# Optimization experiments

Hardware: AMD Instinct MI355X
Metric: run time of the kernel (lower is better)

## Reference

```python
import jax, jax.numpy as jnp
import numpy as np

D_HEAD = 64
KV_HEADS = 8
Q_HEADS = 32
ROPE_BASE = 10000.0


def rope(x):
    # x: (B, S, H, D); pairs are interleaved along last dim, matching torch view(...,D//2,2)
    B, S, H, D = x.shape
    inv_freq = 1.0 / (ROPE_BASE ** (jnp.arange(0, D, 2, dtype=jnp.float32) / D))
    theta = jnp.arange(S, dtype=jnp.float32)[:, None] * inv_freq[None, :]  # (S, D/2)
    cos = jnp.cos(theta)[None, :, None, :]
    sin = jnp.sin(theta)[None, :, None, :]
    xf = x.astype(jnp.float32).reshape(B, S, H, D // 2, 2)
    x1, x2 = xf[..., 0], xf[..., 1]
    out = jnp.stack((x1 * cos - x2 * sin, x1 * sin + x2 * cos), axis=-1)
    return out.reshape(B, S, H, D).astype(x.dtype)


def setup_inputs() -> dict:
    key = jax.random.key(0)
    ks = jax.random.split(key, 5)
    B, S, D = 2, 2048, 2048
    scale = 1.0 / np.sqrt(D)
    return {
        "x": jax.random.normal(ks[0], (B, S, D), dtype=jnp.float32),
        "Wq": jax.random.normal(ks[1], (Q_HEADS * D_HEAD, D), dtype=jnp.float32) * scale,
        "Wk": jax.random.normal(ks[2], (KV_HEADS * D_HEAD, D), dtype=jnp.float32) * scale,
        "Wv": jax.random.normal(ks[3], (KV_HEADS * D_HEAD, D), dtype=jnp.float32) * scale,
        "Wo": jax.random.normal(ks[4], (D, D), dtype=jnp.float32) * scale,
    }


def reference(x, Wq, Wk, Wv, Wo):
    B, S, D = x.shape
    G = Q_HEADS // KV_HEADS  # query heads per kv head

    Q = (x @ Wq.T).reshape(B, S, Q_HEADS, D_HEAD)
    K = (x @ Wk.T).reshape(B, S, KV_HEADS, D_HEAD)
    V = (x @ Wv.T).reshape(B, S, KV_HEADS, D_HEAD)

    Q = rope(Q)
    K = rope(K)

    # (B, KV, G, S, Dh): group g of kv head h corresponds to q head h*G+g,
    # exactly matching repeat_interleave of K/V along head dim.
    Q = Q.transpose(0, 2, 1, 3).reshape(B, KV_HEADS, G, S, D_HEAD)
    K = K.transpose(0, 2, 1, 3)  # (B, KV, S, Dh)
    V = V.transpose(0, 2, 1, 3)

    scores = jnp.einsum("bkgsd,bktd->bkgst", Q, K) / np.sqrt(D_HEAD).astype(np.float32)
    causal_mask = jnp.tril(jnp.ones((S, S), dtype=bool))
    scores = jnp.where(causal_mask, scores, -jnp.inf)
    probs = jax.nn.softmax(scores, axis=-1)
    attn = jnp.einsum("bkgst,bktd->bkgsd", probs, V)

    attn = attn.reshape(B, Q_HEADS, S, D_HEAD).transpose(0, 2, 1, 3).reshape(B, S, D)
    return attn @ Wo.T
```

## Files before the change

### kernel.cpp

```cpp
#include <hip/hip_runtime.h>
#include <stdint.h>

#define S_LEN   2048
#define D_MODEL 2048
#define DKV     512

typedef __attribute__((ext_vector_type(8))) short short8;
typedef __attribute__((ext_vector_type(4))) float f32x4;

__device__ static inline unsigned short f2bf(float f) {
  unsigned u = __builtin_bit_cast(unsigned, f);
  u += 0x7FFFu + ((u >> 16) & 1u);
  return (unsigned short)(u >> 16);
}
__device__ static inline float bf2f(unsigned short h) {
  return __builtin_bit_cast(float, ((unsigned)h) << 16);
}
__device__ static inline unsigned packtrunc2(float f0, float f1) {
  return __builtin_amdgcn_perm(__builtin_bit_cast(unsigned, f1),
                               __builtin_bit_cast(unsigned, f0), 0x07060302u);
}

__device__ static inline void gload_lds16(const void* g, void* lds) {
  __builtin_amdgcn_global_load_lds((const __attribute__((address_space(1))) void*)g,
                                   (__attribute__((address_space(3))) void*)lds,
                                   16, 0, 0);
}

template <int N>
__device__ __forceinline__ void wait_vm() {
  if constexpr (N == 8)      asm volatile("s_waitcnt vmcnt(8)" ::: "memory");
  else if constexpr (N == 6) asm volatile("s_waitcnt vmcnt(6)" ::: "memory");
  else if constexpr (N == 4) asm volatile("s_waitcnt vmcnt(4)" ::: "memory");
  else if constexpr (N == 3) asm volatile("s_waitcnt vmcnt(3)" ::: "memory");
  else                       asm volatile("s_waitcnt vmcnt(0)" ::: "memory");
}

__global__ __launch_bounds__(256) void cvt_all_kernel(
    const float* __restrict__ x, const float* __restrict__ wq, const float* __restrict__ wk,
    const float* __restrict__ wv, const float* __restrict__ wo,
    unsigned short* __restrict__ xb, unsigned short* __restrict__ wqb,
    unsigned short* __restrict__ wkb, unsigned short* __restrict__ wvb,
    unsigned short* __restrict__ wob, float2* __restrict__ tab) {
  if (blockIdx.x >= 9216) {
    const int idx = (blockIdx.x - 9216) * 256 + threadIdx.x;
    const int s = idx >> 5, i = idx & 31;
    const float inv = exp2f(-0.41524101186091903f * (float)i);
    const float th  = (float)s * inv;
    tab[idx] = make_float2(cosf(th), sinf(th));
    return;
  }
  int i = blockIdx.x * 256 + threadIdx.x;
  const float* s; unsigned short* d;
  if (i < 1048576)      { s = x;  d = xb;  }
  else if (i < 1572864) { s = wq; d = wqb; i -= 1048576; }
  else if (i < 1703936) { s = wk; d = wkb; i -= 1572864; }
  else if (i < 1835008) { s = wv; d = wvb; i -= 1703936; }
  else                  { s = wo; d = wob; i -= 1835008; }
  const float4 a = ((const float4*)s)[i * 2];
  const float4 b = ((const float4*)s)[i * 2 + 1];
  unsigned short u[8] = {f2bf(a.x), f2bf(a.y), f2bf(a.z), f2bf(a.w),
                         f2bf(b.x), f2bf(b.y), f2bf(b.z), f2bf(b.w)};
  *(uint4*)(d + (size_t)i * 8) = *(const uint4*)u;
}

template <int BM, int CMODE, int RMODE, typename CT>
__device__ __forceinline__ void gemm_deep_body(
    const unsigned short* __restrict__ A, int lda,
    const unsigned short* __restrict__ B, int ldb,
    CT* __restrict__ C, int ldc, int m0, int n0, unsigned short* ldsu,
    const float2* __restrict__ tab) {
  constexpr int MI = BM / 32;
  constexpr int NI = 4;
  constexpr int A_BYTES = BM * 64;
  constexpr int B_BYTES = 256 * 64;
  constexpr int TILE_BYTES = A_BYTES + B_BYTES;
  constexpr int AL = BM / 128;
  constexpr int LOADS = AL + 2;
  constexpr int VMS = 2 * LOADS;

  const int tid  = threadIdx.x;
  const int lane = tid & 63;
  const int w    = tid >> 6;
  const int wm   = w >> 2;
  const int wn   = w & 3;
  const int lcol = lane & 15;
  const int lq   = lane >> 4;
  char* const ldsb = (char*)ldsu;

  const int sl   = (lane & 7) ^ (lane >> 3);
  const int colg = (sl & 3) * 8;
  const unsigned short* gA[AL];
  const unsigned short* gB[2];
#pragma unroll
  for (int L = 0; L < AL; ++L) {
    const int r = 2 * (L * 64 + w * 8 + (lane >> 3)) + (sl >> 2);
    gA[L] = A + (size_t)(m0 + r) * lda + colg;
  }
#pragma unroll
  for (int L = 0; L < 2; ++L) {
    const int r = 2 * (L * 64 + w * 8 + (lane >> 3)) + (sl >> 2);
    gB[L] = B + (size_t)(n0 + r) * ldb + colg;
  }

  auto stage = [&](int tt) {
    char* const sb = ldsb + (tt & 3) * TILE_BYTES;
#pragma unroll
    for (int L = 0; L < AL; ++L)
      gload_lds16(gA[L] + tt * 32, sb + L * 8192 + w * 1024);
#pragma unroll
    for (int L = 0; L < 2; ++L)
      gload_lds16(gB[L] + tt * 32, sb + A_BYTES + L * 8192 + w * 1024);
  };

  const int sR    = (((lcol & 1) << 2) | lq) ^ ((lcol >> 1) & 7);
  const int rdoff = (lcol >> 1) * 128 + sR * 16;

  f32x4 acc[MI][NI] = {};

  auto compute_tile = [&](char* buf) {
    short8 af[MI], bfr[NI];
#pragma unroll
    for (int mi = 0; mi < MI; ++mi)
      af[mi] = *(const short8*)(buf + wm * (MI * 1024) + mi * 1024 + rdoff);
#pragma unroll
    for (int ni = 0; ni < NI; ++ni)
      bfr[ni] = *(const short8*)(buf + A_BYTES + wn * 4096 + ni * 1024 + rdoff);
    __builtin_amdgcn_s_setprio(1);
#pragma unroll
    for (int mi = 0; mi < MI; ++mi)
#pragma unroll
      for (int ni = 0; ni < NI; ++ni)
        acc[mi][ni] = __builtin_amdgcn_mfma_f32_16x16x32_bf16(af[mi], bfr[ni], acc[mi][ni], 0, 0, 0);
    __builtin_amdgcn_s_setprio(0);
  };

  stage(0); stage(1); stage(2);

#define GPHASE(T, VMW, DOSTG)                          \
  do {                                                 \
    wait_vm<VMW>();                                    \
    __builtin_amdgcn_s_barrier();                      \
    asm volatile("" ::: "memory");                     \
    __builtin_amdgcn_sched_barrier(0);                 \
    if (DOSTG) stage((T) + 3);                         \
    compute_tile(ldsb + ((T) & 3) * TILE_BYTES);       \
  } while (0)

  for (int t4 = 0; t4 < 15; ++t4) {
    const int t = t4 * 4;
    GPHASE(t + 0, VMS, true);
    GPHASE(t + 1, VMS, true);
    GPHASE(t + 2, VMS, true);
    GPHASE(t + 3, VMS, true);
  }
  GPHASE(60, VMS,   true);
  GPHASE(61, VMS,   false);
  GPHASE(62, LOADS, false);
  GPHASE(63, 0,     false);
#undef GPHASE

  if constexpr (CMODE == 1) {
    unsigned short* ldsT = ldsu;
    __syncthreads();
#pragma unroll
    for (int mi = 0; mi < MI; ++mi)
#pragma unroll
      for (int ni = 0; ni < NI; ++ni) {
        const int c  = wn * 64 + ni * 16 + lcol;
        const int rl = wm * (MI * 16) + mi * 16 + lq * 4;
        unsigned short u4[4] = {f2bf(acc[mi][ni][0]), f2bf(acc[mi][ni][1]),
                                f2bf(acc[mi][ni][2]), f2bf(acc[mi][ni][3])};
        *(uint2*)&ldsT[c * 264 + rl] = *(const uint2*)u4;
      }
    __syncthreads();
    const int bI   = m0 >> 11;
    const int s0   = m0 & 2047;
    const int half = lane >> 5;
    const int sl32 = lane & 31;
#pragma unroll
    for (int it = 0; it < 16; ++it) {
      const int d = it * 16 + w * 2 + half;
      const uint4 v = *(const uint4*)&ldsT[d * 264 + sl32 * 8];
      *(uint4*)&C[((size_t)(bI * 512 + n0 + d)) * 2048 + s0 + sl32 * 8] = v;
    }
  } else {
#pragma unroll
    for (int mi = 0; mi < MI; ++mi)
#pragma unroll
      for (int ni = 0; ni < NI; ++ni)
#pragma unroll
        for (int r = 0; r < 4; ++r) {
          const int row = m0 + wm * (MI * 16) + mi * 16 + lq * 4 + r;
          const int col = n0 + wn * 64 + ni * 16 + lcol;
          float v = acc[mi][ni][r];
          if constexpr (RMODE > 0) {
            const float p = __shfl_xor(v, 1);
            const int d = col & 63;
            const float2 cs = tab[(row & (S_LEN - 1)) * 32 + (d >> 1)];
            v = (d & 1) ? (p * cs.y + v * cs.x) : (v * cs.x - p * cs.y);
            if constexpr (RMODE == 2) v *= 0.1803368801111244f;
          }
          if constexpr (CMODE == 2) {
            C[(size_t)row * ldc + col] = v;
          } else {
            C[(size_t)row * ldc + col] = f2bf(v);
          }
        }
  }
}

__global__ __launch_bounds__(512, 2) void qkv_gemm_kernel(
    const unsigned short* __restrict__ x,
    const unsigned short* __restrict__ Wq, const unsigned short* __restrict__ Wk,
    const unsigned short* __restrict__ Wv,
    unsigned short* __restrict__ Qo, unsigned short* __restrict__ Ko,
    unsigned short* __restrict__ Vt, const float2* __restrict__ tab) {
  extern __shared__ __align__(16) unsigned short lds[];
  const int bid = blockIdx.x;
  const int xcd = bid & 7, l = bid >> 3;
  const int gm = xcd >> 2, gn = xcd & 3;
  const int mt = gm * 8 + (l & 7);
  const int nt = gn * 3 + (l >> 3);
  const int m0 = mt * 256;
  if (nt < 8)
    gemm_deep_body<256, 0, 2, unsigned short>(x, D_MODEL, Wq, D_MODEL, Qo, D_MODEL, m0, nt * 256, lds, tab);
  else if (nt < 10)
    gemm_deep_body<256, 0, 1, unsigned short>(x, D_MODEL, Wk, D_MODEL, Ko, DKV, m0, (nt - 8) * 256, lds, tab);
  else
    gemm_deep_body<256, 1, 0, unsigned short>(x, D_MODEL, Wv, D_MODEL, Vt, DKV, m0, (nt - 10) * 256, lds, tab);
}

__global__ __launch_bounds__(512, 2) void oproj_gemm_kernel(
    const unsigned short* __restrict__ A, const unsigned short* __restrict__ Wo,
    float* __restrict__ C) {
  extern __shared__ __align__(16) unsigned short lds[];
  const int bid = blockIdx.x;
  const int xcd = bid & 7, l = bid >> 3;
  const int gm = xcd >> 1, gn = xcd & 1;
  const int mt = gm * 8 + (l & 7);
  const int nt = gn * 4 + (l >> 3);
  gemm_deep_body<128, 2, 0, float>(A, D_MODEL, Wo, D_MODEL, C, D_MODEL, mt * 128, nt * 256, lds,
                                   (const float2*)nullptr);
}

__global__ __launch_bounds__(256, 2) void attn_kernel(const unsigned short* __restrict__ Q,
                                                      const unsigned short* __restrict__ K,
                                                      const unsigned short* __restrict__ Vt,
                                                      unsigned short* __restrict__ O) {
  const int hq = blockIdx.y;
  const int bb = blockIdx.z;
  const int hk = hq >> 2;
  const int tid  = threadIdx.x;
  const int lane = tid & 63;
  const int w    = tid >> 6;
  const int lcol = lane & 15;
  const int lq   = lane >> 4;
  const int trow = tid >> 2;
  const int tq   = (tid & 3) * 16;

  const int X = blockIdx.x;
  const int qt[4] = {X, 15 - X, 16 + X, 31 - X};

  __shared__ unsigned short Ks[64 * 72];
  __shared__ unsigned short Vts[64 * 72];
  __shared__ unsigned short Ps[4][64 * 72];

  const int prow = w * 16 + lcol;

  uint4 kp0, kp1, vp0, vp1;
  {
    const unsigned short* gk = K + ((size_t)(bb * S_LEN + trow)) * DKV + hk * 64 + tq;
    kp0 = *(const uint4*)gk; kp1 = *(const uint4*)(gk + 8);
    const unsigned short* gv = Vt + ((size_t)(bb * DKV + hk * 64 + trow)) * S_LEN + tq;
    vp0 = *(const uint4*)gv; vp1 = *(const uint4*)(gv + 8);
  }

#pragma unroll
  for (int j = 0; j < 4; ++j) {
    const unsigned short* g = Q + ((size_t)(bb * S_LEN + qt[j] * 64 + trow)) * D_MODEL + hq * 64 + tq;
    *(uint4*)&Ps[j][trow * 72 + tq]     = *(const uint4*)g;
    *(uint4*)&Ps[j][trow * 72 + tq + 8] = *(const uint4*)(g + 8);
  }
  asm volatile("s_waitcnt lgkmcnt(0)" ::: "memory");

  short8 qf[4][2];
#pragma unroll
  for (int j = 0; j < 4; ++j)
#pragma unroll
    for (int ks = 0; ks < 2; ++ks)
      qf[j][ks] = *(const short8*)&Ps[j][prow * 72 + ks * 32 + lq * 8];

  f32x4 Oacc[4][4] = {};
  float lacc[4] = {0.f, 0.f, 0.f, 0.f};

  const int tmax = qt[3];
  for (int t = 0; t <= tmax; ++t) {
    __syncthreads();
    *(uint4*)&Ks[trow * 72 + tq]      = kp0;
    *(uint4*)&Ks[trow * 72 + tq + 8]  = kp1;
    *(uint4*)&Vts[trow * 72 + tq]     = vp0;
    *(uint4*)&Vts[trow * 72 + tq + 8] = vp1;
    if (t < tmax) {
      const int t1 = (t + 1) * 64;
      const unsigned short* gk = K + ((size_t)(bb * S_LEN + t1 + trow)) * DKV + hk * 64 + tq;
      kp0 = *(const uint4*)gk; kp1 = *(const uint4*)(gk + 8);
      const unsigned short* gv = Vt + ((size_t)(bb * DKV + hk * 64 + trow)) * S_LEN + t1 + tq;
      vp0 = *(const uint4*)gv; vp1 = *(const uint4*)(gv + 8);
    }
    __syncthreads();

    bool act[4];
#pragma unroll
    for (int j = 0; j < 4; ++j) act[j] = (t <= qt[j]);

    f32x4 S[4][4] = {};
#pragma unroll
    for (int ks = 0; ks < 2; ++ks)
#pragma unroll
      for (int nt = 0; nt < 4; ++nt) {
        const short8 kf = *(const short8*)&Ks[(nt * 16 + lcol) * 72 + ks * 32 + lq * 8];
#pragma unroll
        for (int j = 0; j < 4; ++j)
          if (act[j])
            S[j][nt] = __builtin_amdgcn_mfma_f32_16x16x32_bf16(kf, qf[j][ks], S[j][nt], 0, 0, 0);
      }

#pragma unroll
    for (int j = 0; j < 4; ++j) {
      if (!act[j]) continue;
      if (t == qt[j]) {
        const int qrow = qt[j] * 64 + prow;
#pragma unroll
        for (int nt = 0; nt < 4; ++nt)
#pragma unroll
          for (int r = 0; r < 4; ++r) {
            const int key = t * 64 + nt * 16 + lq * 4 + r;
            if (key > qrow) S[j][nt][r] = -1e30f;
          }
      }
#pragma unroll
      for (int nt = 0; nt < 4; ++nt) {
        const float p0 = __builtin_amdgcn_exp2f(S[j][nt][0]);
        const float p1 = __builtin_amdgcn_exp2f(S[j][nt][1]);
        const float p2 = __builtin_amdgcn_exp2f(S[j][nt][2]);
        const float p3 = __builtin_amdgcn_exp2f(S[j][nt][3]);
        lacc[j] += (p0 + p1) + (p2 + p3);
        unsigned u2[2] = {packtrunc2(p0, p1), packtrunc2(p2, p3)};
        *(uint2*)&Ps[j][prow * 72 + nt * 16 + lq * 4] = *(const uint2*)u2;
      }
    }
    asm volatile("s_waitcnt lgkmcnt(0)" ::: "memory");

#pragma unroll
    for (int ks = 0; ks < 2; ++ks) {
      short8 pf[4];
#pragma unroll
      for (int j = 0; j < 4; ++j)
        if (act[j]) pf[j] = *(const short8*)&Ps[j][prow * 72 + ks * 32 + lq * 8];
#pragma unroll
      for (int dt = 0; dt < 4; ++dt) {
        const short8 vf = *(const short8*)&Vts[(dt * 16 + lcol) * 72 + ks * 32 + lq * 8];
#pragma unroll
        for (int j = 0; j < 4; ++j)
          if (act[j])
            Oacc[j][dt] = __builtin_amdgcn_mfma_f32_16x16x32_bf16(vf, pf[j], Oacc[j][dt], 0, 0, 0);
      }
    }
  }

#pragma unroll
  for (int j = 0; j < 4; ++j) {
    float l = lacc[j];
    l += __shfl_xor(l, 16);
    l += __shfl_xor(l, 32);
    const float inv = 1.0f / l;
    const int qrow = qt[j] * 64 + prow;
#pragma unroll
    for (int dt = 0; dt < 4; ++dt) {
      unsigned short u[4] = {f2bf(Oacc[j][dt][0] * inv), f2bf(Oacc[j][dt][1] * inv),
                             f2bf(Oacc[j][dt][2] * inv), f2bf(Oacc[j][dt][3] * inv)};
      *(uint2*)&O[(size_t)(bb * S_LEN + qrow) * D_MODEL + hq * 64 + dt * 16 + lq * 4] =
          *(const uint2*)u;
    }
  }
}

extern "C" void kernel_launch(void* const* d_in, const int* in_sizes, int n_in,
                              void* d_out, int out_size, void* d_ws, size_t ws_size,
                              hipStream_t stream) {
  const float* x  = (const float*)d_in[0];
  const float* Wq = (const float*)d_in[1];
  const float* Wk = (const float*)d_in[2];
  const float* Wv = (const float*)d_in[3];
  const float* Wo = (const float*)d_in[4];
  float* out = (float*)d_out;

  unsigned short* Qb  = (unsigned short*)d_ws;
  unsigned short* Kb  = Qb  + (size_t)4096 * 2048;
  unsigned short* Vtg = Kb  + (size_t)4096 * 512;
  unsigned short* Ab  = Vtg + (size_t)1024 * 2048;
  unsigned short* xb  = Ab  + (size_t)4096 * 2048;
  unsigned short* Wqb = xb  + (size_t)4096 * 2048;
  unsigned short* Wkb = Wqb + (size_t)2048 * 2048;
  unsigned short* Wvb = Wkb + (size_t)512 * 2048;
  unsigned short* Wob = Wvb + (size_t)512 * 2048;
  float2* tab = (float2*)(Wob + (size_t)2048 * 2048);

  static bool attr_set = false;
  if (!attr_set) {
    hipFuncSetAttribute(reinterpret_cast<const void*>(qkv_gemm_kernel),
                        hipFuncAttributeMaxDynamicSharedMemorySize, 135168);
    hipFuncSetAttribute(reinterpret_cast<const void*>(oproj_gemm_kernel),
                        hipFuncAttributeMaxDynamicSharedMemorySize, 98304);
    attr_set = true;
  }

  cvt_all_kernel<<<9472, 256, 0, stream>>>(x, Wq, Wk, Wv, Wo, xb, Wqb, Wkb, Wvb, Wob, tab);

  qkv_gemm_kernel<<<192, 512, 135168, stream>>>(xb, Wqb, Wkb, Wvb, Qb, Kb, Vtg, tab);
  attn_kernel<<<dim3(8, 32, 2), 256, 0, stream>>>(Qb, Kb, Vtg, Ab);
  oproj_gemm_kernel<<<256, 512, 98304, stream>>>(Ab, Wob, out);
}
```

Measured before the change: 275.4 us.

## Shrink QKV and O-proj GEMM tiles to 128x128 with 256-thread blocks

Replaces the 256x256 (QKV) and 128x256 (O-proj) GEMM tiles with one 128x128 tile specialisation using 4 waves and 64 KB of LDS. It launches 768 and 512 blocks instead of 192 and 256, and remaps the XCD-aware block swizzle to match. The goal is to fill all CUs of the MI355X, since the old grids left many idle, and to let more blocks co-reside. In exchange, each K-slice gets less data reuse, which means more global and LDS traffic per FLOP.

Result: slower. 283.0 us (+2.8%).

```diff
diff --git a/kernel.cpp b/kernel.cpp
--- a/kernel.cpp
+++ b/kernel.cpp
@@ -64,73 +64,61 @@
   *(uint4*)(d + (size_t)i * 8) = *(const uint4*)u;
 }
 
-template <int BM, int CMODE, int RMODE, typename CT>
-__device__ __forceinline__ void gemm_deep_body(
+template <int CMODE, int RMODE, typename CT>
+__device__ __forceinline__ void gemm128_deep(
     const unsigned short* __restrict__ A, int lda,
     const unsigned short* __restrict__ B, int ldb,
-    CT* __restrict__ C, int ldc, int m0, int n0, unsigned short* ldsu,
-    const float2* __restrict__ tab) {
-  constexpr int MI = BM / 32;
-  constexpr int NI = 4;
-  constexpr int A_BYTES = BM * 64;
-  constexpr int B_BYTES = 256 * 64;
-  constexpr int TILE_BYTES = A_BYTES + B_BYTES;
-  constexpr int AL = BM / 128;
-  constexpr int LOADS = AL + 2;
-  constexpr int VMS = 2 * LOADS;
-
+    CT* __restrict__ C, int ldc, int m0, int n0,
+    unsigned short* ldsu, const float2* __restrict__ tab) {
+  constexpr int LOADS = 4;
+  constexpr int VMS   = 8;
   const int tid  = threadIdx.x;
   const int lane = tid & 63;
   const int w    = tid >> 6;
-  const int wm   = w >> 2;
-  const int wn   = w & 3;
+  const int wm   = w >> 1, wn = w & 1;
   const int lcol = lane & 15;
   const int lq   = lane >> 4;
   char* const ldsb = (char*)ldsu;
 
   const int sl   = (lane & 7) ^ (lane >> 3);
   const int colg = (sl & 3) * 8;
-  const unsigned short* gA[AL];
+  const unsigned short* gA[2];
   const unsigned short* gB[2];
 #pragma unroll
-  for (int L = 0; L < AL; ++L) {
-    const int r = 2 * (L * 64 + w * 8 + (lane >> 3)) + (sl >> 2);
+  for (int L = 0; L < 2; ++L) {
+    const int r = 2 * (L * 32 + w * 8 + (lane >> 3)) + (sl >> 2);
     gA[L] = A + (size_t)(m0 + r) * lda + colg;
-  }
-#pragma unroll
-  for (int L = 0; L < 2; ++L) {
-    const int r = 2 * (L * 64 + w * 8 + (lane >> 3)) + (sl >> 2);
     gB[L] = B + (size_t)(n0 + r) * ldb + colg;
   }
 
   auto stage = [&](int tt) {
-    char* const sb = ldsb + (tt & 3) * TILE_BYTES;
-#pragma unroll
-    for (int L = 0; L < AL; ++L)
-      gload_lds16(gA[L] + tt * 32, sb + L * 8192 + w * 1024);
+    char* const sb = ldsb + (tt & 3) * 16384;
 #pragma unroll
     for (int L = 0; L < 2; ++L)
-      gload_lds16(gB[L] + tt * 32, sb + A_BYTES + L * 8192 + w * 1024);
+      gload_lds16(gA[L] + tt * 32, sb + L * 4096 + w * 1024);
+#pragma unroll
+    for (int L = 0; L < 2; ++L)
+      gload_lds16(gB[L] + tt * 32, sb + 8192 + L * 4096 + w * 1024);
   };
 
   const int sR    = (((lcol & 1) << 2) | lq) ^ ((lcol >> 1) & 7);
   const int rdoff = (lcol >> 1) * 128 + sR * 16;
 
-  f32x4 acc[MI][NI] = {};
+  f32x4 acc[4][4] = {};
 
   auto compute_tile = [&](char* buf) {
-    short8 af[MI], bfr[NI];
-#pragma unroll
-    for (int mi = 0; mi < MI; ++mi)
-      af[mi] = *(const short8*)(buf + wm * (MI * 1024) + mi * 1024 + rdoff);
-#pragma unroll
-    for (int ni = 0; ni < NI; ++ni)
-      bfr[ni] = *(const short8*)(buf + A_BYTES + wn * 4096 + ni * 1024 + rdoff);
+    short8 af[4], bfr[4];
+#pragma unroll
+    for (int mi = 0; mi < 4; ++mi)
+      af[mi] = *(const short8*)(buf + wm * 4096 + mi * 1024 + rdoff);
+#pragma unroll
+    for (int ni = 0; ni < 4; ++ni)
+      bfr[ni] = *(const short8*)(buf + 8192 + wn * 4096 + ni * 1024 + rdoff);
     __builtin_amdgcn_s_setprio(1);
 #pragma unroll
-    for (int mi = 0; mi < MI; ++mi)
-#pragma unroll
-      for (int ni = 0; ni < NI; ++ni)
+    for (int mi = 0; mi < 4; ++mi)
+#pragma unroll
+      for (int ni = 0; ni < 4; ++ni)
         acc[mi][ni] = __builtin_amdgcn_mfma_f32_16x16x32_bf16(af[mi], bfr[ni], acc[mi][ni], 0, 0, 0);
     __builtin_amdgcn_s_setprio(0);
   };
@@ -144,7 +132,7 @@
     asm volatile("" ::: "memory");                     \
     __builtin_amdgcn_sched_barrier(0);                 \
     if (DOSTG) stage((T) + 3);                         \
-    compute_tile(ldsb + ((T) & 3) * TILE_BYTES);       \
+    compute_tile(ldsb + ((T) & 3) * 16384);            \
   } while (0)
 
   for (int t4 = 0; t4 < 15; ++t4) {
@@ -164,34 +152,32 @@
     unsigned short* ldsT = ldsu;
     __syncthreads();
 #pragma unroll
-    for (int mi = 0; mi < MI; ++mi)
-#pragma unroll
-      for (int ni = 0; ni < NI; ++ni) {
+    for (int mi = 0; mi < 4; ++mi)
+#pragma unroll
+      for (int ni = 0; ni < 4; ++ni) {
         const int c  = wn * 64 + ni * 16 + lcol;
-        const int rl = wm * (MI * 16) + mi * 16 + lq * 4;
+        const int rl = wm * 64 + mi * 16 + lq * 4;
         unsigned short u4[4] = {f2bf(acc[mi][ni][0]), f2bf(acc[mi][ni][1]),
                                 f2bf(acc[mi][ni][2]), f2bf(acc[mi][ni][3])};
-        *(uint2*)&ldsT[c * 264 + rl] = *(const uint2*)u4;
+        *(uint2*)&ldsT[c * 136 + rl] = *(const uint2*)u4;
       }
     __syncthreads();
-    const int bI   = m0 >> 11;
-    const int s0   = m0 & 2047;
-    const int half = lane >> 5;
-    const int sl32 = lane & 31;
-#pragma unroll
-    for (int it = 0; it < 16; ++it) {
-      const int d = it * 16 + w * 2 + half;
-      const uint4 v = *(const uint4*)&ldsT[d * 264 + sl32 * 8];
-      *(uint4*)&C[((size_t)(bI * 512 + n0 + d)) * 2048 + s0 + sl32 * 8] = v;
+    const int bI = m0 >> 11;
+    const int s0 = m0 & 2047;
+#pragma unroll
+    for (int it = 0; it < 8; ++it) {
+      const int d = it * 16 + (tid >> 4);
+      *(uint4*)&C[((size_t)(bI * 512 + n0 + d)) * 2048 + s0 + (tid & 15) * 8] =
+          *(const uint4*)&ldsT[d * 136 + (tid & 15) * 8];
     }
   } else {
 #pragma unroll
-    for (int mi = 0; mi < MI; ++mi)
-#pragma unroll
-      for (int ni = 0; ni < NI; ++ni)
+    for (int mi = 0; mi < 4; ++mi)
+#pragma unroll
+      for (int ni = 0; ni < 4; ++ni)
 #pragma unroll
         for (int r = 0; r < 4; ++r) {
-          const int row = m0 + wm * (MI * 16) + mi * 16 + lq * 4 + r;
+          const int row = m0 + wm * 64 + mi * 16 + lq * 4 + r;
           const int col = n0 + wn * 64 + ni * 16 + lcol;
           float v = acc[mi][ni][r];
           if constexpr (RMODE > 0) {
@@ -210,7 +196,7 @@
   }
 }
 
-__global__ __launch_bounds__(512, 2) void qkv_gemm_kernel(
+__global__ __launch_bounds__(256) void qkv_gemm_kernel(
     const unsigned short* __restrict__ x,
     const unsigned short* __restrict__ Wq, const unsigned short* __restrict__ Wk,
     const unsigned short* __restrict__ Wv,
@@ -219,29 +205,27 @@
   extern __shared__ __align__(16) unsigned short lds[];
   const int bid = blockIdx.x;
   const int xcd = bid & 7, l = bid >> 3;
-  const int gm = xcd >> 2, gn = xcd & 3;
-  const int mt = gm * 8 + (l & 7);
-  const int nt = gn * 3 + (l >> 3);
-  const int m0 = mt * 256;
-  if (nt < 8)
-    gemm_deep_body<256, 0, 2, unsigned short>(x, D_MODEL, Wq, D_MODEL, Qo, D_MODEL, m0, nt * 256, lds, tab);
-  else if (nt < 10)
-    gemm_deep_body<256, 0, 1, unsigned short>(x, D_MODEL, Wk, D_MODEL, Ko, DKV, m0, (nt - 8) * 256, lds, tab);
+  const int mt = (xcd >> 2) * 16 + (l & 15);
+  const int nt = (xcd & 3) * 6 + (l >> 4);
+  const int m0 = mt * 128;
+  if (nt < 16)
+    gemm128_deep<0, 2, unsigned short>(x, D_MODEL, Wq, D_MODEL, Qo, D_MODEL, m0, nt * 128, lds, tab);
+  else if (nt < 20)
+    gemm128_deep<0, 1, unsigned short>(x, D_MODEL, Wk, D_MODEL, Ko, DKV, m0, (nt - 16) * 128, lds, tab);
   else
-    gemm_deep_body<256, 1, 0, unsigned short>(x, D_MODEL, Wv, D_MODEL, Vt, DKV, m0, (nt - 10) * 256, lds, tab);
-}
-
-__global__ __launch_bounds__(512, 2) void oproj_gemm_kernel(
+    gemm128_deep<1, 0, unsigned short>(x, D_MODEL, Wv, D_MODEL, Vt, DKV, m0, (nt - 20) * 128, lds, tab);
+}
+
+__global__ __launch_bounds__(256) void oproj_gemm_kernel(
     const unsigned short* __restrict__ A, const unsigned short* __restrict__ Wo,
     float* __restrict__ C) {
   extern __shared__ __align__(16) unsigned short lds[];
   const int bid = blockIdx.x;
   const int xcd = bid & 7, l = bid >> 3;
-  const int gm = xcd >> 1, gn = xcd & 1;
-  const int mt = gm * 8 + (l & 7);
-  const int nt = gn * 4 + (l >> 3);
-  gemm_deep_body<128, 2, 0, float>(A, D_MODEL, Wo, D_MODEL, C, D_MODEL, mt * 128, nt * 256, lds,
-                                   (const float2*)nullptr);
+  const int mt = (xcd >> 2) * 16 + (l & 15);
+  const int nt = (xcd & 3) * 4 + (l >> 4);
+  gemm128_deep<2, 0, float>(A, D_MODEL, Wo, D_MODEL, C, D_MODEL, mt * 128, nt * 128, lds,
+                            (const float2*)nullptr);
 }
 
 __global__ __launch_bounds__(256, 2) void attn_kernel(const unsigned short* __restrict__ Q,
@@ -410,15 +394,15 @@
   static bool attr_set = false;
   if (!attr_set) {
     hipFuncSetAttribute(reinterpret_cast<const void*>(qkv_gemm_kernel),
-                        hipFuncAttributeMaxDynamicSharedMemorySize, 135168);
+                        hipFuncAttributeMaxDynamicSharedMemorySize, 65536);
     hipFuncSetAttribute(reinterpret_cast<const void*>(oproj_gemm_kernel),
-                        hipFuncAttributeMaxDynamicSharedMemorySize, 98304);
+                        hipFuncAttributeMaxDynamicSharedMemorySize, 65536);
     attr_set = true;
   }
 
   cvt_all_kernel<<<9472, 256, 0, stream>>>(x, Wq, Wk, Wv, Wo, xb, Wqb, Wkb, Wvb, Wob, tab);
 
-  qkv_gemm_kernel<<<192, 512, 135168, stream>>>(xb, Wqb, Wkb, Wvb, Qb, Kb, Vtg, tab);
+  qkv_gemm_kernel<<<768, 256, 65536, stream>>>(xb, Wqb, Wkb, Wvb, Qb, Kb, Vtg, tab);
   attn_kernel<<<dim3(8, 32, 2), 256, 0, stream>>>(Qb, Kb, Vtg, Ab);
-  oproj_gemm_kernel<<<256, 512, 98304, stream>>>(Ab, Wob, out);
-}
+  oproj_gemm_kernel<<<512, 256, 65536, stream>>>(Ab, Wob, out);
+}
```
